# Kernel tuning notes

Hardware: AMD Instinct MI355X
Metric: run time of the kernel (lower is better)

The kernel has to match this reference:

```python
import jax, jax.numpy as jnp
import numpy as np

N, E, D, H, C, L = 50000, 600000, 128, 128, 40, 2
NEG_SLOPE = 0.1


def setup_inputs() -> dict:
    key = jax.random.key(0)
    ks = jax.random.split(key, 12)

    def lin(k, din, dout):
        return (jax.random.normal(k, (din, dout), jnp.float32) / np.sqrt(din)).astype(jnp.float32)

    x = jax.random.normal(ks[0], (N, D), jnp.float32)
    edge_index = jax.random.randint(ks[1], (2, E), 0, N, dtype=jnp.int32)
    return {
        "x": x,
        "edge_index": edge_index,
        "enc_Wl": lin(ks[2], D, H),
        "enc_Wr": lin(ks[3], D, H),
        "enc_b": jnp.zeros((H,), jnp.float32),
        "lay_Wl": jnp.stack([lin(jax.random.fold_in(ks[4], i), H, H) for i in range(L)]),
        "lay_Wr": jnp.stack([lin(jax.random.fold_in(ks[5], i), H, H) for i in range(L)]),
        "lay_b": jnp.zeros((L, H), jnp.float32),
        "dec_Wl": lin(ks[6], H, C),
        "dec_Wr": lin(ks[7], H, C),
        "dec_b": jnp.zeros((C,), jnp.float32),
    }


def _sage(x, src, dst, inv_cnt, Wl, Wr, b):
    # mean-aggregate neighbor messages: gather x[src], scatter-sum to dst, divide by degree
    agg = jax.ops.segment_sum(x[src], dst, num_segments=N) * inv_cnt  # [N, d_in]
    return agg @ Wl + x @ Wr + b


def reference(x, edge_index, enc_Wl, enc_Wr, enc_b, lay_Wl, lay_Wr, lay_b, dec_Wl, dec_Wr, dec_b):
    src, dst = edge_index[0], edge_index[1]
    # in-degree per target node, clamped to 1 (PyG scatter-mean semantics: isolated nodes get 0)
    deg = jax.ops.segment_sum(jnp.ones((E,), jnp.float32), dst, num_segments=N)
    inv_cnt = (1.0 / jnp.maximum(deg, 1.0))[:, None]  # [N, 1]

    h = jax.nn.leaky_relu(_sage(x, src, dst, inv_cnt, enc_Wl, enc_Wr, enc_b), NEG_SLOPE)
    for i in range(L):
        h = jax.nn.leaky_relu(_sage(h, src, dst, inv_cnt, lay_Wl[i], lay_Wr[i], lay_b[i]), NEG_SLOPE)
    out = _sage(h, src, dst, inv_cnt, dec_Wl, dec_Wr, dec_b)
    return jax.nn.log_softmax(out, axis=1)
```

## Files before the change

### kernel.cpp

```cpp
#include <hip/hip_runtime.h>
#include <hip/hip_bf16.h>

#define NN 50000
#define EE 600000
#define HH 128
#define CC 40
#define NEG 0.1f
#define CAP 40

typedef __attribute__((ext_vector_type(8))) short bf16x8;
typedef __attribute__((ext_vector_type(4))) float f32x4;

__device__ __forceinline__ unsigned short f2bf(float f) {
    unsigned u = __float_as_uint(f);
    unsigned r = u + 0x7fffu + ((u >> 16) & 1u);
    return (unsigned short)(r >> 16);
}
__device__ __forceinline__ float bfhi(unsigned v) { return __uint_as_float(v & 0xFFFF0000u); }
__device__ __forceinline__ float bflo(unsigned v) { return __uint_as_float(v << 16); }

__global__ void k_build(const int* __restrict__ src, const int* __restrict__ dst,
                        int* __restrict__ counts, int* __restrict__ csr) {
    int e = blockIdx.x * blockDim.x + threadIdx.x;
    if (e < EE) {
        int d = dst[e];
        if ((unsigned)d < (unsigned)NN) {
            int sl = atomicAdd(&counts[d], 1);
            if (sl < CAP) csr[d * CAP + sl] = src[e];
        }
    }
}

struct PrepArgs {
    const float* wsrc[8];
    unsigned short* wdst[8];
    int* counts;
    const float* x;
    unsigned* xb;
};

template <int DOUT, int DOUTP>
__device__ __forceinline__ void swz_one(const float* __restrict__ W,
                                        unsigned short* __restrict__ dstf, int idx) {
    int k = idx / DOUTP, n = idx % DOUTP;
    unsigned short val = (n < DOUT) ? f2bf(W[k * DOUT + n]) : (unsigned short)0;
    int kt = k >> 5, kin = k & 31, nt = n >> 4, nin = n & 15;
    int lane = ((kin >> 3) << 4) | nin;
    int j = kin & 7;
    int NT = DOUTP >> 4;
    dstf[(((kt * NT + nt) * 64) + lane) * 8 + j] = val;
}

__global__ void k_prep(PrepArgs a) {
    int b = blockIdx.x;
    if (b < 384) {
        int tid = b * 256 + threadIdx.x;
        if (tid < NN) a.counts[tid] = 0;
        int which = b >> 6;
        int idx = (b & 63) * 256 + threadIdx.x;
        swz_one<HH, HH>(a.wsrc[which], a.wdst[which], idx);
    } else if (b < 432) {
        int bb = b - 384;
        int which = 6 + bb / 24;
        int idx = (bb % 24) * 256 + threadIdx.x;
        swz_one<CC, 48>(a.wsrc[which], a.wdst[which], idx);
    } else {
        int t = (b - 432) * 256 + threadIdx.x;
        if (t < NN * HH / 4) {
            float4 v = ((const float4*)a.x)[t];
            uint2 o;
            o.x = ((unsigned)f2bf(v.y) << 16) | f2bf(v.x);
            o.y = ((unsigned)f2bf(v.w) << 16) | f2bf(v.z);
            ((uint2*)a.xb)[t] = o;
        }
    }
}

template <int MODE>
__global__ __launch_bounds__(1024, 8) void k_layer(
    const unsigned short* __restrict__ hin,
    const int* __restrict__ counts, const int* __restrict__ csr,
    const unsigned short* __restrict__ B1f, const unsigned short* __restrict__ B2f,
    const float* __restrict__ bias, unsigned short* __restrict__ out,
    const unsigned short* __restrict__ Tf, unsigned short* __restrict__ tOut) {
    __shared__ unsigned lds[16][72];
    int wid = threadIdx.x >> 6;
    int lane = threadIdx.x & 63;
    int m0 = blockIdx.x * 16;
    int gg = lane & 15;
    int s = lane >> 4;
    const uint4* hw4 = (const uint4*)hin;

    int node = m0 + wid;
    int cnt = counts[node];
    cnt = cnt < CAP ? cnt : CAP;
    int beg = node * CAP;
    float sc = 1.0f / (float)(cnt > 0 ? cnt : 1);
    int sr = (__builtin_amdgcn_readfirstlane(cnt) + 3) >> 2;

    int row[10];
#pragma unroll
    for (int r = 0; r < 10; ++r) {
        int v = csr[beg + r * 4 + s];
        row[r] = ((unsigned)v < (unsigned)NN) ? v : 0;
    }

    float acc[8];
#pragma unroll
    for (int d = 0; d < 8; ++d) acc[d] = 0.f;

    uint4 vA, vB, vC;

#define ISS(R, V) \
    if (sr > (R)) V = hw4[((unsigned)row[R] << 4) + gg]
#define ACC8(R, V)                                            \
    if (sr > (R)) {                                           \
        if ((R) * 4 + s < cnt) {                              \
            acc[0] += bflo(V.x); acc[1] += bfhi(V.x);         \
            acc[2] += bflo(V.y); acc[3] += bfhi(V.y);         \
            acc[4] += bflo(V.z); acc[5] += bfhi(V.z);         \
            acc[6] += bflo(V.w); acc[7] += bfhi(V.w);         \
        }                                                     \
    }

    ISS(0, vA); ISS(1, vB); ISS(2, vC);
    ACC8(0, vA); ISS(3, vA);
    ACC8(1, vB); ISS(4, vB);
    ACC8(2, vC); ISS(5, vC);
    ACC8(3, vA); ISS(6, vA);
    ACC8(4, vB); ISS(7, vB);
    ACC8(5, vC); ISS(8, vC);
    ACC8(6, vA); ISS(9, vA);
    ACC8(7, vB);
    ACC8(8, vC);
    ACC8(9, vA);
#undef ISS
#undef ACC8

#pragma unroll
    for (int d = 0; d < 8; ++d) {
        float t = acc[d];
        t += __shfl_xor(t, 16, 64);
        t += __shfl_xor(t, 32, 64);
        acc[d] = t * sc;
    }
    if (lane < 16) {
        uint4 w4;
        w4.x = ((unsigned)f2bf(acc[1]) << 16) | f2bf(acc[0]);
        w4.y = ((unsigned)f2bf(acc[3]) << 16) | f2bf(acc[2]);
        w4.z = ((unsigned)f2bf(acc[5]) << 16) | f2bf(acc[4]);
        w4.w = ((unsigned)f2bf(acc[7]) << 16) | f2bf(acc[6]);
        *(uint4*)&lds[wid][gg * 4] = w4;
    }
    __syncthreads();

    int nin = lane & 15;
    int kq = lane >> 4;
    unsigned short hv[4];

    if (wid < 8) {
        const unsigned* arow = &lds[nin][0];
        f32x4 acc1 = (f32x4){0.f, 0.f, 0.f, 0.f};

#pragma unroll
        for (int kt = 0; kt < 4; ++kt) {
            bf16x8 a1 = *(const bf16x8*)(arow + kt * 16 + kq * 4);
            bf16x8 a2 = *(const bf16x8*)(hin + (size_t)(m0 + nin) * HH + kt * 32 + kq * 8);
            bf16x8 b1 = *(const bf16x8*)(B1f + (((kt * 8 + wid) * 64) + lane) * 8);
            acc1 = __builtin_amdgcn_mfma_f32_16x16x32_bf16(a1, b1, acc1, 0, 0, 0);
            bf16x8 b2 = *(const bf16x8*)(B2f + (((kt * 8 + wid) * 64) + lane) * 8);
            acc1 = __builtin_amdgcn_mfma_f32_16x16x32_bf16(a2, b2, acc1, 0, 0, 0);
        }

        int col = wid * 16 + nin;
        float bv = bias[col];
#pragma unroll
        for (int r = 0; r < 4; ++r) {
            int m = m0 + kq * 4 + r;
            float v = acc1[r] + bv;
            v = fmaxf(v, NEG * v);
            hv[r] = f2bf(v);
            out[(size_t)m * HH + col] = hv[r];
        }
    }

    if (MODE == 1) {
        __syncthreads();
        unsigned short* lsh = (unsigned short*)&lds[0][0];
        if (wid < 8) {
            int col = wid * 16 + nin;
#pragma unroll
            for (int r = 0; r < 4; ++r) lsh[(kq * 4 + r) * 144 + col] = hv[r];
        }
        __syncthreads();
        if (wid < 3) {
            f32x4 at = (f32x4){0.f, 0.f, 0.f, 0.f};
#pragma unroll
            for (int kt = 0; kt < 4; ++kt) {
                bf16x8 a = *(const bf16x8*)&lsh[nin * 144 + kt * 32 + kq * 8];
                bf16x8 b = *(const bf16x8*)(Tf + (((kt * 3 + wid) * 64) + lane) * 8);
                at = __builtin_amdgcn_mfma_f32_16x16x32_bf16(a, b, at, 0, 0, 0);
            }
#pragma unroll
            for (int r = 0; r < 4; ++r) {
                int m = m0 + kq * 4 + r;
                tOut[(size_t)m * 48 + wid * 16 + nin] = f2bf(at[r]);
            }
        }
    }
}

__global__ __launch_bounds__(1024, 8) void k_dec(
    const unsigned short* __restrict__ tbuf,
    const unsigned short* __restrict__ h1,
    const int* __restrict__ counts, const int* __restrict__ csr,
    const unsigned short* __restrict__ B2f, const float* __restrict__ bias,
    float* __restrict__ out) {
    __shared__ float aggT[16][52];
    int wid = threadIdx.x >> 6;
    int lane = threadIdx.x & 63;
    int m0 = blockIdx.x * 16;
    int g = lane & 7;
    int g6 = g < 6 ? g : g - 6;
    int s = lane >> 3;
    const uint4* t4 = (const uint4*)tbuf;

    int node = m0 + wid;
    int cnt = counts[node];
    cnt = cnt < CAP ? cnt : CAP;
    int beg = node * CAP;
    float sc = 1.0f / (float)(cnt > 0 ? cnt : 1);
    int sr = (__builtin_amdgcn_readfirstlane(cnt) + 7) >> 3;

    int row[5];
#pragma unroll
    for (int r = 0; r < 5; ++r) {
        int v = csr[beg + r * 8 + s];
        row[r] = ((unsigned)v < (unsigned)NN) ? v : 0;
    }

    float acc[8];
#pragma unroll
    for (int d = 0; d < 8; ++d) acc[d] = 0.f;

    uint4 vA, vB, vC;

#define ISSD(R, V) \
    if (sr > (R)) V = t4[(unsigned)row[R] * 6 + g6]
#define ACCD(R, V)                                            \
    if (sr > (R)) {                                           \
        if ((R) * 8 + s < cnt) {                              \
            acc[0] += bflo(V.x); acc[1] += bfhi(V.x);         \
            acc[2] += bflo(V.y); acc[3] += bfhi(V.y);         \
            acc[4] += bflo(V.z); acc[5] += bfhi(V.z);         \
            acc[6] += bflo(V.w); acc[7] += bfhi(V.w);         \
        }                                                     \
    }

    ISSD(0, vA); ISSD(1, vB); ISSD(2, vC);
    ACCD(0, vA); ISSD(3, vA);
    ACCD(1, vB); ISSD(4, vB);
    ACCD(2, vC);
    ACCD(3, vA);
    ACCD(4, vB);
#undef ISSD
#undef ACCD

#pragma unroll
    for (int d = 0; d < 8; ++d) {
        float t = acc[d];
        t += __shfl_xor(t, 8, 64);
        t += __shfl_xor(t, 16, 64);
        t += __shfl_xor(t, 32, 64);
        acc[d] = t * sc;
    }
    if (s == 0 && g < 6) {
        float4 p0, p1;
        p0.x = acc[0]; p0.y = acc[1]; p0.z = acc[2]; p0.w = acc[3];
        p1.x = acc[4]; p1.y = acc[5]; p1.z = acc[6]; p1.w = acc[7];
        *(float4*)&aggT[wid][8 * g] = p0;
        *(float4*)&aggT[wid][8 * g + 4] = p1;
    }
    __syncthreads();
    if (wid != 0) return;

    int nin = lane & 15, kq = lane >> 4;
    f32x4 acc2[3];
#pragma unroll
    for (int j = 0; j < 3; ++j) acc2[j] = (f32x4){0.f, 0.f, 0.f, 0.f};
#pragma unroll
    for (int kt = 0; kt < 4; ++kt) {
        bf16x8 a2 = *(const bf16x8*)(h1 + (size_t)(m0 + nin) * HH + kt * 32 + kq * 8);
#pragma unroll
        for (int j = 0; j < 3; ++j) {
            bf16x8 b2 = *(const bf16x8*)(B2f + (((kt * 3 + j) * 64) + lane) * 8);
            acc2[j] = __builtin_amdgcn_mfma_f32_16x16x32_bf16(a2, b2, acc2[j], 0, 0, 0);
        }
    }
    float bv[3];
#pragma unroll
    for (int t = 0; t < 3; ++t) {
        int col = t * 16 + nin;
        bv[t] = (col < CC) ? bias[col] : 0.f;
    }
#pragma unroll
    for (int r = 0; r < 4; ++r) {
        int m = m0 + kq * 4 + r;
        int ml = kq * 4 + r;
        float v[3];
        float mx = -1e30f;
#pragma unroll
        for (int t = 0; t < 3; ++t) {
            int col = t * 16 + nin;
            v[t] = acc2[t][r] + aggT[ml][col] + bv[t];
            if (col < CC) mx = fmaxf(mx, v[t]);
        }
        for (int off = 1; off < 16; off <<= 1) mx = fmaxf(mx, __shfl_xor(mx, off, 64));
        float sm = 0.f;
#pragma unroll
        for (int t = 0; t < 3; ++t) {
            int col = t * 16 + nin;
            if (col < CC) sm += expf(v[t] - mx);
        }
        for (int off = 1; off < 16; off <<= 1) sm += __shfl_xor(sm, off, 64);
        float lse = mx + logf(sm);
#pragma unroll
        for (int t = 0; t < 3; ++t) {
            int col = t * 16 + nin;
            if (col < CC) out[(size_t)m * CC + col] = v[t] - lse;
        }
    }
}

extern "C" void kernel_launch(void* const* d_in, const int* in_sizes, int n_in,
                              void* d_out, int out_size, void* d_ws, size_t ws_size,
                              hipStream_t stream) {
    const float* x      = (const float*)d_in[0];
    const int*   ei     = (const int*)d_in[1];
    const float* enc_Wl = (const float*)d_in[2];
    const float* enc_Wr = (const float*)d_in[3];
    const float* enc_b  = (const float*)d_in[4];
    const float* lay_Wl = (const float*)d_in[5];
    const float* lay_Wr = (const float*)d_in[6];
    const float* lay_b  = (const float*)d_in[7];
    const float* dec_Wl = (const float*)d_in[8];
    const float* dec_Wr = (const float*)d_in[9];
    const float* dec_b  = (const float*)d_in[10];
    float* out = (float*)d_out;

    const int* src = ei;
    const int* dst = ei + EE;

    char* p = (char*)d_ws;
    auto carve = [&](size_t bytes) {
        char* r = p;
        p += (bytes + 255) & ~(size_t)255;
        return r;
    };
    int*            counts = (int*)carve(NN * 4);
    int*            csr    = (int*)carve((size_t)NN * CAP * 4);
    unsigned short* h1     = (unsigned short*)carve((size_t)NN * HH * 2);
    unsigned short* h2     = (unsigned short*)carve((size_t)NN * HH * 2);
    unsigned short* tbuf   = (unsigned short*)carve((size_t)NN * 48 * 2 + 256);
    unsigned short* wf[8];
    for (int i = 0; i < 6; ++i) wf[i] = (unsigned short*)carve(HH * HH * 2);
    wf[6] = (unsigned short*)carve(HH * 48 * 2);
    wf[7] = (unsigned short*)carve(HH * 48 * 2);

    {
        PrepArgs a;
        a.wsrc[0] = enc_Wl; a.wsrc[1] = enc_Wr;
        a.wsrc[2] = lay_Wl; a.wsrc[3] = lay_Wr;
        a.wsrc[4] = lay_Wl + HH * HH; a.wsrc[5] = lay_Wr + HH * HH;
        a.wsrc[6] = dec_Wl; a.wsrc[7] = dec_Wr;
        for (int i = 0; i < 8; ++i) a.wdst[i] = wf[i];
        a.counts = counts;
        a.x = x;
        a.xb = (unsigned*)h2;
        k_prep<<<432 + (NN * HH / 4 + 255) / 256, 256, 0, stream>>>(a);
    }

    k_build<<<(EE + 255) / 256, 256, 0, stream>>>(src, dst, counts, csr);

    const int FB = NN / 16;
    k_layer<0><<<FB, 1024, 0, stream>>>(h2, counts, csr, wf[0], wf[1], enc_b,      h1, nullptr, nullptr);
    k_layer<0><<<FB, 1024, 0, stream>>>(h1, counts, csr, wf[2], wf[3], lay_b,      h2, nullptr, nullptr);
    k_layer<1><<<FB, 1024, 0, stream>>>(h2, counts, csr, wf[4], wf[5], lay_b + HH, h1, wf[6], tbuf);

    k_dec<<<FB, 1024, 0, stream>>>(tbuf, h1, counts, csr, wf[7], dec_b, out);
}
```

Before: 295.7 us.

## Bucket nodes by degree via permutation and specialize gather depth per wave

```diff
diff --git a/kernel.cpp b/kernel.cpp
--- a/kernel.cpp
+++ b/kernel.cpp
@@ -7,6 +7,8 @@
 #define CC 40
 #define NEG 0.1f
 #define CAP 40
+#define NSLOT 50176
+#define NBLK (NSLOT / 16)
 
 typedef __attribute__((ext_vector_type(8))) short bf16x8;
 typedef __attribute__((ext_vector_type(4))) float f32x4;
@@ -31,12 +33,48 @@
     }
 }
 
+__global__ void k_hist(const int* __restrict__ counts, int* __restrict__ hist) {
+    __shared__ int lh[16];
+    if (threadIdx.x < 16) lh[threadIdx.x] = 0;
+    __syncthreads();
+    int n = blockIdx.x * 256 + threadIdx.x;
+    if (n < NN) {
+        int c = counts[n]; c = c < CAP ? c : CAP;
+        atomicAdd(&lh[(c + 3) >> 2], 1);
+    }
+    __syncthreads();
+    if (threadIdx.x < 11) atomicAdd(&hist[threadIdx.x], lh[threadIdx.x]);
+}
+
+__global__ void k_prefix(const int* __restrict__ hist, int* __restrict__ base) {
+    if (threadIdx.x == 0) {
+        int acc = 0;
+        for (int r = 10; r >= 0; --r) {
+            base[r] = acc;
+            acc += (hist[r] + 15) & ~15;
+        }
+    }
+}
+
+__global__ void k_place(const int* __restrict__ counts, const int* __restrict__ base,
+                        int* __restrict__ fill, unsigned* __restrict__ perm) {
+    int n = blockIdx.x * 256 + threadIdx.x;
+    if (n < NN) {
+        int c = counts[n]; c = c < CAP ? c : CAP;
+        int r = (c + 3) >> 2;
+        int slot = base[r] + atomicAdd(&fill[r], 1);
+        if (slot >= 0 && slot < NSLOT) perm[slot] = (unsigned)n | ((unsigned)c << 16);
+    }
+}
+
 struct PrepArgs {
     const float* wsrc[8];
     unsigned short* wdst[8];
     int* counts;
     const float* x;
     unsigned* xb;
+    unsigned* perm;
+    int* aux;
 };
 
 template <int DOUT, int DOUTP>
@@ -50,6 +88,9 @@
     int NT = DOUTP >> 4;
     dstf[(((kt * NT + nt) * 64) + lane) * 8 + j] = val;
 }
+
+#define XCB ((NN * HH / 4 + 255) / 256)
+#define PFB ((NSLOT + 255) / 256)
 
 __global__ void k_prep(PrepArgs a) {
     int b = blockIdx.x;
@@ -64,7 +105,7 @@
         int which = 6 + bb / 24;
         int idx = (bb % 24) * 256 + threadIdx.x;
         swz_one<CC, 48>(a.wsrc[which], a.wdst[which], idx);
-    } else {
+    } else if (b < 432 + XCB) {
         int t = (b - 432) * 256 + threadIdx.x;
         if (t < NN * HH / 4) {
             float4 v = ((const float4*)a.x)[t];
@@ -73,17 +114,47 @@
             o.y = ((unsigned)f2bf(v.w) << 16) | f2bf(v.z);
             ((uint2*)a.xb)[t] = o;
         }
+    } else {
+        int i = (b - (432 + XCB)) * 256 + threadIdx.x;
+        if (i < NSLOT) a.perm[i] = 0xFFFFFFFFu;
+        if (i < 64) a.aux[i] = 0;
+    }
+}
+
+template <int R>
+__device__ __forceinline__ void gather_batch(const int* __restrict__ crow,
+                                             const uint4* __restrict__ hw4,
+                                             int s, int gg, int cnt, int base_r,
+                                             float (&acc)[8]) {
+    int rv[R]; uint4 vb[R];
+#pragma unroll
+    for (int r = 0; r < R; ++r) rv[r] = crow[(base_r + r) * 4 + s];
+#pragma unroll
+    for (int r = 0; r < R; ++r) {
+        unsigned rw = ((unsigned)rv[r] < (unsigned)NN) ? (unsigned)rv[r] : 0u;
+        vb[r] = hw4[(size_t)rw * 16 + gg];
+    }
+#pragma unroll
+    for (int r = 0; r < R; ++r) {
+        if ((base_r + r) * 4 + s < cnt) {
+            acc[0] += bflo(vb[r].x); acc[1] += bfhi(vb[r].x);
+            acc[2] += bflo(vb[r].y); acc[3] += bfhi(vb[r].y);
+            acc[4] += bflo(vb[r].z); acc[5] += bfhi(vb[r].z);
+            acc[6] += bflo(vb[r].w); acc[7] += bfhi(vb[r].w);
+        }
     }
 }
 
 template <int MODE>
 __global__ __launch_bounds__(1024, 8) void k_layer(
     const unsigned short* __restrict__ hin,
-    const int* __restrict__ counts, const int* __restrict__ csr,
+    const unsigned* __restrict__ perm,
+    const int* __restrict__ csr,
     const unsigned short* __restrict__ B1f, const unsigned short* __restrict__ B2f,
     const float* __restrict__ bias, unsigned short* __restrict__ out,
     const unsigned short* __restrict__ Tf, unsigned short* __restrict__ tOut) {
     __shared__ unsigned lds[16][72];
+    __shared__ int nodeTab[16];
     int wid = threadIdx.x >> 6;
     int lane = threadIdx.x & 63;
     int m0 = blockIdx.x * 16;
@@ -91,51 +162,39 @@
     int s = lane >> 4;
     const uint4* hw4 = (const uint4*)hin;
 
-    int node = m0 + wid;
-    int cnt = counts[node];
-    cnt = cnt < CAP ? cnt : CAP;
-    int beg = node * CAP;
-    float sc = 1.0f / (float)(cnt > 0 ? cnt : 1);
-    int sr = (__builtin_amdgcn_readfirstlane(cnt) + 3) >> 2;
-
-    int row[10];
-#pragma unroll
-    for (int r = 0; r < 10; ++r) {
-        int v = csr[beg + r * 4 + s];
-        row[r] = ((unsigned)v < (unsigned)NN) ? v : 0;
-    }
+    unsigned pe = perm[m0 + wid];
+    int pes = __builtin_amdgcn_readfirstlane((int)pe);
+    int node = pes & 0xffff;
+    int cnt = (pes >> 16) & 0xffff;
+    int valid = node < NN;
+    if (lane == 0) nodeTab[wid] = valid ? node : (1 << 30);
+    int rounds = valid ? (cnt + 3) >> 2 : 0;
+    rounds = rounds < 10 ? rounds : 10;
+    float sc = 1.0f / (float)((valid && cnt > 0) ? cnt : 1);
+    const int* crow = csr + (size_t)(valid ? node : 0) * CAP;
 
     float acc[8];
 #pragma unroll
     for (int d = 0; d < 8; ++d) acc[d] = 0.f;
 
-    uint4 vA, vB, vC;
-
-#define ISS(R, V) \
-    if (sr > (R)) V = hw4[((unsigned)row[R] << 4) + gg]
-#define ACC8(R, V)                                            \
-    if (sr > (R)) {                                           \
-        if ((R) * 4 + s < cnt) {                              \
-            acc[0] += bflo(V.x); acc[1] += bfhi(V.x);         \
-            acc[2] += bflo(V.y); acc[3] += bfhi(V.y);         \
-            acc[4] += bflo(V.z); acc[5] += bfhi(V.z);         \
-            acc[6] += bflo(V.w); acc[7] += bfhi(V.w);         \
-        }                                                     \
-    }
-
-    ISS(0, vA); ISS(1, vB); ISS(2, vC);
-    ACC8(0, vA); ISS(3, vA);
-    ACC8(1, vB); ISS(4, vB);
-    ACC8(2, vC); ISS(5, vC);
-    ACC8(3, vA); ISS(6, vA);
-    ACC8(4, vB); ISS(7, vB);
-    ACC8(5, vC); ISS(8, vC);
-    ACC8(6, vA); ISS(9, vA);
-    ACC8(7, vB);
-    ACC8(8, vC);
-    ACC8(9, vA);
-#undef ISS
-#undef ACC8
+    switch (rounds) {
+        case 0: break;
+        case 1: gather_batch<1>(crow, hw4, s, gg, cnt, 0, acc); break;
+        case 2: gather_batch<2>(crow, hw4, s, gg, cnt, 0, acc); break;
+        case 3: gather_batch<3>(crow, hw4, s, gg, cnt, 0, acc); break;
+        case 4: gather_batch<4>(crow, hw4, s, gg, cnt, 0, acc); break;
+        case 5: gather_batch<5>(crow, hw4, s, gg, cnt, 0, acc); break;
+        case 6: gather_batch<3>(crow, hw4, s, gg, cnt, 0, acc);
+                gather_batch<3>(crow, hw4, s, gg, cnt, 3, acc); break;
+        case 7: gather_batch<4>(crow, hw4, s, gg, cnt, 0, acc);
+                gather_batch<3>(crow, hw4, s, gg, cnt, 4, acc); break;
+        case 8: gather_batch<4>(crow, hw4, s, gg, cnt, 0, acc);
+                gather_batch<4>(crow, hw4, s, gg, cnt, 4, acc); break;
+        case 9: gather_batch<5>(crow, hw4, s, gg, cnt, 0, acc);
+                gather_batch<4>(crow, hw4, s, gg, cnt, 5, acc); break;
+        default: gather_batch<5>(crow, hw4, s, gg, cnt, 0, acc);
+                 gather_batch<5>(crow, hw4, s, gg, cnt, 5, acc); break;
+    }
 
 #pragma unroll
     for (int d = 0; d < 8; ++d) {
@@ -160,12 +219,14 @@
 
     if (wid < 8) {
         const unsigned* arow = &lds[nin][0];
+        int node2 = nodeTab[nin];
+        int na = node2 < NN ? node2 : 0;
         f32x4 acc1 = (f32x4){0.f, 0.f, 0.f, 0.f};
 
 #pragma unroll
         for (int kt = 0; kt < 4; ++kt) {
             bf16x8 a1 = *(const bf16x8*)(arow + kt * 16 + kq * 4);
-            bf16x8 a2 = *(const bf16x8*)(hin + (size_t)(m0 + nin) * HH + kt * 32 + kq * 8);
+            bf16x8 a2 = *(const bf16x8*)(hin + (size_t)na * HH + kt * 32 + kq * 8);
             bf16x8 b1 = *(const bf16x8*)(B1f + (((kt * 8 + wid) * 64) + lane) * 8);
             acc1 = __builtin_amdgcn_mfma_f32_16x16x32_bf16(a1, b1, acc1, 0, 0, 0);
             bf16x8 b2 = *(const bf16x8*)(B2f + (((kt * 8 + wid) * 64) + lane) * 8);
@@ -176,11 +237,11 @@
         float bv = bias[col];
 #pragma unroll
         for (int r = 0; r < 4; ++r) {
-            int m = m0 + kq * 4 + r;
             float v = acc1[r] + bv;
             v = fmaxf(v, NEG * v);
             hv[r] = f2bf(v);
-            out[(size_t)m * HH + col] = hv[r];
+            int nm = nodeTab[kq * 4 + r];
+            if (nm < NN) out[(size_t)nm * HH + col] = hv[r];
         }
     }
 
@@ -203,9 +264,32 @@
             }
 #pragma unroll
             for (int r = 0; r < 4; ++r) {
-                int m = m0 + kq * 4 + r;
-                tOut[(size_t)m * 48 + wid * 16 + nin] = f2bf(at[r]);
+                int nm = nodeTab[kq * 4 + r];
+                if (nm < NN) tOut[(size_t)nm * 48 + wid * 16 + nin] = f2bf(at[r]);
             }
+        }
+    }
+}
+
+template <int R>
+__device__ __forceinline__ void gatherd_batch(const int* __restrict__ crow,
+                                              const uint4* __restrict__ t4,
+                                              int s, int g6, int cnt, float (&acc)[8]) {
+    int rv[R]; uint4 vb[R];
+#pragma unroll
+    for (int r = 0; r < R; ++r) rv[r] = crow[r * 8 + s];
+#pragma unroll
+    for (int r = 0; r < R; ++r) {
+        unsigned rw = ((unsigned)rv[r] < (unsigned)NN) ? (unsigned)rv[r] : 0u;
+        vb[r] = t4[(size_t)rw * 6 + g6];
+    }
+#pragma unroll
+    for (int r = 0; r < R; ++r) {
+        if (r * 8 + s < cnt) {
+            acc[0] += bflo(vb[r].x); acc[1] += bfhi(vb[r].x);
+            acc[2] += bflo(vb[r].y); acc[3] += bfhi(vb[r].y);
+            acc[4] += bflo(vb[r].z); acc[5] += bfhi(vb[r].z);
+            acc[6] += bflo(vb[r].w); acc[7] += bfhi(vb[r].w);
         }
     }
 }
@@ -213,10 +297,12 @@
 __global__ __launch_bounds__(1024, 8) void k_dec(
     const unsigned short* __restrict__ tbuf,
     const unsigned short* __restrict__ h1,
-    const int* __restrict__ counts, const int* __restrict__ csr,
+    const unsigned* __restrict__ perm,
+    const int* __restrict__ csr,
     const unsigned short* __restrict__ B2f, const float* __restrict__ bias,
     float* __restrict__ out) {
     __shared__ float aggT[16][52];
+    __shared__ int nodeTab[16];
     int wid = threadIdx.x >> 6;
     int lane = threadIdx.x & 63;
     int m0 = blockIdx.x * 16;
@@ -225,46 +311,29 @@
     int s = lane >> 3;
     const uint4* t4 = (const uint4*)tbuf;
 
-    int node = m0 + wid;
-    int cnt = counts[node];
-    cnt = cnt < CAP ? cnt : CAP;
-    int beg = node * CAP;
-    float sc = 1.0f / (float)(cnt > 0 ? cnt : 1);
-    int sr = (__builtin_amdgcn_readfirstlane(cnt) + 7) >> 3;
-
-    int row[5];
-#pragma unroll
-    for (int r = 0; r < 5; ++r) {
-        int v = csr[beg + r * 8 + s];
-        row[r] = ((unsigned)v < (unsigned)NN) ? v : 0;
-    }
+    unsigned pe = perm[m0 + wid];
+    int pes = __builtin_amdgcn_readfirstlane((int)pe);
+    int node = pes & 0xffff;
+    int cnt = (pes >> 16) & 0xffff;
+    int valid = node < NN;
+    if (lane == 0) nodeTab[wid] = valid ? node : (1 << 30);
+    int rounds = valid ? (cnt + 7) >> 3 : 0;
+    rounds = rounds < 5 ? rounds : 5;
+    float sc = 1.0f / (float)((valid && cnt > 0) ? cnt : 1);
+    const int* crow = csr + (size_t)(valid ? node : 0) * CAP;
 
     float acc[8];
 #pragma unroll
     for (int d = 0; d < 8; ++d) acc[d] = 0.f;
 
-    uint4 vA, vB, vC;
-
-#define ISSD(R, V) \
-    if (sr > (R)) V = t4[(unsigned)row[R] * 6 + g6]
-#define ACCD(R, V)                                            \
-    if (sr > (R)) {                                           \
-        if ((R) * 8 + s < cnt) {                              \
-            acc[0] += bflo(V.x); acc[1] += bfhi(V.x);         \
-            acc[2] += bflo(V.y); acc[3] += bfhi(V.y);         \
-            acc[4] += bflo(V.z); acc[5] += bfhi(V.z);         \
-            acc[6] += bflo(V.w); acc[7] += bfhi(V.w);         \
-        }                                                     \
-    }
-
-    ISSD(0, vA); ISSD(1, vB); ISSD(2, vC);
-    ACCD(0, vA); ISSD(3, vA);
-    ACCD(1, vB); ISSD(4, vB);
-    ACCD(2, vC);
-    ACCD(3, vA);
-    ACCD(4, vB);
-#undef ISSD
-#undef ACCD
+    switch (rounds) {
+        case 0: break;
+        case 1: gatherd_batch<1>(crow, t4, s, g6, cnt, acc); break;
+        case 2: gatherd_batch<2>(crow, t4, s, g6, cnt, acc); break;
+        case 3: gatherd_batch<3>(crow, t4, s, g6, cnt, acc); break;
+        case 4: gatherd_batch<4>(crow, t4, s, g6, cnt, acc); break;
+        default: gatherd_batch<5>(crow, t4, s, g6, cnt, acc); break;
+    }
 
 #pragma unroll
     for (int d = 0; d < 8; ++d) {
@@ -285,12 +354,14 @@
     if (wid != 0) return;
 
     int nin = lane & 15, kq = lane >> 4;
+    int node2 = nodeTab[nin];
+    int na = node2 < NN ? node2 : 0;
     f32x4 acc2[3];
 #pragma unroll
     for (int j = 0; j < 3; ++j) acc2[j] = (f32x4){0.f, 0.f, 0.f, 0.f};
 #pragma unroll
     for (int kt = 0; kt < 4; ++kt) {
-        bf16x8 a2 = *(const bf16x8*)(h1 + (size_t)(m0 + nin) * HH + kt * 32 + kq * 8);
+        bf16x8 a2 = *(const bf16x8*)(h1 + (size_t)na * HH + kt * 32 + kq * 8);
 #pragma unroll
         for (int j = 0; j < 3; ++j) {
             bf16x8 b2 = *(const bf16x8*)(B2f + (((kt * 3 + j) * 64) + lane) * 8);
@@ -305,8 +376,8 @@
     }
 #pragma unroll
     for (int r = 0; r < 4; ++r) {
-        int m = m0 + kq * 4 + r;
         int ml = kq * 4 + r;
+        int nm = nodeTab[ml];
         float v[3];
         float mx = -1e30f;
 #pragma unroll
@@ -327,7 +398,7 @@
 #pragma unroll
         for (int t = 0; t < 3; ++t) {
             int col = t * 16 + nin;
-            if (col < CC) out[(size_t)m * CC + col] = v[t] - lse;
+            if (col < CC && nm < NN) out[(size_t)nm * CC + col] = v[t] - lse;
         }
     }
 }
@@ -362,6 +433,8 @@
     unsigned short* h1     = (unsigned short*)carve((size_t)NN * HH * 2);
     unsigned short* h2     = (unsigned short*)carve((size_t)NN * HH * 2);
     unsigned short* tbuf   = (unsigned short*)carve((size_t)NN * 48 * 2 + 256);
+    unsigned*       perm   = (unsigned*)carve((size_t)NSLOT * 4);
+    int*            aux    = (int*)carve(64 * 4);
     unsigned short* wf[8];
     for (int i = 0; i < 6; ++i) wf[i] = (unsigned short*)carve(HH * HH * 2);
     wf[6] = (unsigned short*)carve(HH * 48 * 2);
@@ -377,15 +450,19 @@
         a.counts = counts;
         a.x = x;
         a.xb = (unsigned*)h2;
-        k_prep<<<432 + (NN * HH / 4 + 255) / 256, 256, 0, stream>>>(a);
+        a.perm = perm;
+        a.aux = aux;
+        k_prep<<<432 + XCB + PFB, 256, 0, stream>>>(a);
     }
 
     k_build<<<(EE + 255) / 256, 256, 0, stream>>>(src, dst, counts, csr);
-
-    const int FB = NN / 16;
-    k_layer<0><<<FB, 1024, 0, stream>>>(h2, counts, csr, wf[0], wf[1], enc_b,      h1, nullptr, nullptr);
-    k_layer<0><<<FB, 1024, 0, stream>>>(h1, counts, csr, wf[2], wf[3], lay_b,      h2, nullptr, nullptr);
-    k_layer<1><<<FB, 1024, 0, stream>>>(h2, counts, csr, wf[4], wf[5], lay_b + HH, h1, wf[6], tbuf);
-
-    k_dec<<<FB, 1024, 0, stream>>>(tbuf, h1, counts, csr, wf[7], dec_b, out);
-}
+    k_hist<<<(NN + 255) / 256, 256, 0, stream>>>(counts, aux);
+    k_prefix<<<1, 64, 0, stream>>>(aux, aux + 32);
+    k_place<<<(NN + 255) / 256, 256, 0, stream>>>(counts, aux + 32, aux + 16, perm);
+
+    k_layer<0><<<NBLK, 1024, 0, stream>>>(h2, perm, csr, wf[0], wf[1], enc_b,      h1, nullptr, nullptr);
+    k_layer<0><<<NBLK, 1024, 0, stream>>>(h1, perm, csr, wf[2], wf[3], lay_b,      h2, nullptr, nullptr);
+    k_layer<1><<<NBLK, 1024, 0, stream>>>(h2, perm, csr, wf[4], wf[5], lay_b + HH, h1, wf[6], tbuf);
+
+    k_dec<<<NBLK, 1024, 0, stream>>>(tbuf, h1, perm, csr, wf[7], dec_b, out);
+}
```

After: 616.0 us. +108.3%, slower.
